# Optimization experiments

Hardware: AMD Instinct MI355X
Metric: run time of the kernel (lower is better)

Reference implementation:

```python
import jax, jax.numpy as jnp
import numpy as np

TEMPERATURE = 0.07
BASE_TEMPERATURE = 0.07


def setup_inputs() -> dict:
    key = jax.random.key(0)
    k1, k2 = jax.random.split(key)
    N, D = 8192, 512
    features = jax.random.normal(k1, (N, D), dtype=jnp.float32)
    labels = jax.random.randint(k2, (N,), 0, 64, dtype=jnp.int64 if jax.config.jax_enable_x64 else jnp.int32)
    return {"features": features, "labels": labels, "rotation_multiplier": 2}


def reference(features, labels, rotation_multiplier):
    k = int(rotation_multiplier)
    N = features.shape[0]
    B = N // k
    # L2-normalize rows (torch F.normalize clamps norm at eps=1e-12)
    norm = jnp.maximum(jnp.linalg.norm(features, axis=1, keepdims=True), 1e-12)
    f = features / norm
    sim = jnp.matmul(f, f.T) / TEMPERATURE  # [N, N]

    # block positive mask: groups of k rows share a label; compare group labels
    lab = labels.reshape(B, k)[:, 0]  # [B]
    same = lab[:, None] == lab[None, :]  # [B, B]
    mask = jnp.repeat(jnp.repeat(same, k, axis=0), k, axis=1)  # [N, N]
    eye = jnp.eye(N, dtype=bool)
    mask = mask & ~eye

    # stable masked log-softmax with diagonal removed from denominator
    logits_max = jax.lax.stop_gradient(jnp.max(sim, axis=1, keepdims=True))
    logits = sim - logits_max
    exp_logits = jnp.exp(logits)
    denom = exp_logits.sum(axis=1, keepdims=True) - jnp.diagonal(exp_logits)[:, None] + 1e-8
    log_prob = logits - jnp.log(denom)

    mask_f = mask.astype(logits.dtype)
    mask_sum = mask_f.sum(axis=1)  # [N]
    valid = mask_sum > 0
    mean_log_prob_pos = (log_prob * mask_f).sum(axis=1) / jnp.maximum(mask_sum, 1.0)
    per_sample = -(TEMPERATURE / BASE_TEMPERATURE) * mean_log_prob_pos
    n_valid = valid.sum().astype(logits.dtype)
    loss = jnp.where(valid, per_sample, 0.0).sum() / jnp.maximum(n_valid, 1.0)
    return loss
```

## Files before the change

kernel.cpp:

```cpp
#include <hip/hip_runtime.h>
#include <hip/hip_bf16.h>

#define TEMP_INV 14.285714285714286f
#define FSCALE 16.0f
#define T1S (TEMP_INV / 256.0f)

typedef __attribute__((ext_vector_type(4))) float f32x4;

#define ASYNC_COPY16(gp, lp)                                                  \
  __builtin_amdgcn_global_load_lds(                                           \
      (__attribute__((address_space(1))) const void*)(gp),                    \
      (__attribute__((address_space(3))) void*)(lp), 16, 0, 0)

__global__ __launch_bounds__(256) void norm_label_k(const float* __restrict__ feat,
                                                    uchar* __restrict__ fq,
                                                    const int* __restrict__ labels,
                                                    const int* __restrict__ kptr,
                                                    int* __restrict__ glab,
                                                    int* __restrict__ cnt,
                                                    float* __restrict__ gacc,
                                                    int* __restrict__ dcnt,
                                                    int N, int D) {
  const int row = (blockIdx.x * 256 + threadIdx.x) >> 6;
  const int lane = threadIdx.x & 63;
  if (row < N) {
    const float4* fr = (const float4*)(feat + (size_t)row * D);
    float4 v0 = fr[lane * 2];
    float4 v1 = fr[lane * 2 + 1];
    float ss = v0.x * v0.x + v0.y * v0.y + v0.z * v0.z + v0.w * v0.w +
               v1.x * v1.x + v1.y * v1.y + v1.z * v1.z + v1.w * v1.w;
    #pragma unroll
    for (int off = 32; off; off >>= 1) ss += __shfl_xor(ss, off, 64);
    const float inv = FSCALE / fmaxf(sqrtf(ss), 1e-12f);
    int w0 = 0, w1 = 0;
    w0 = __builtin_amdgcn_cvt_pk_fp8_f32(v0.x * inv, v0.y * inv, w0, false);
    w0 = __builtin_amdgcn_cvt_pk_fp8_f32(v0.z * inv, v0.w * inv, w0, true);
    w1 = __builtin_amdgcn_cvt_pk_fp8_f32(v1.x * inv, v1.y * inv, w1, false);
    w1 = __builtin_amdgcn_cvt_pk_fp8_f32(v1.z * inv, v1.w * inv, w1, true);
    uint2 o; o.x = (uint)w0; o.y = (uint)w1;
    *(uint2*)(fq + (size_t)row * D + lane * 8) = o;
  }
  if (blockIdx.x == 0) {
    const int k = *kptr;
    const int B = N / k;
    __shared__ int h[64];
    const int t = threadIdx.x;
    if (t < 2) gacc[t] = 0.f;
    if (t == 2) *dcnt = 0;
    if (t < 64) h[t] = 0;
    __syncthreads();
    for (int b = t; b < B; b += 256) {
      int lb = labels[(size_t)b * k];
      if (lb >= 0 && lb < 64) atomicAdd(&h[lb], 1);
    }
    __syncthreads();
    if (t < 64) cnt[t] = h[t];
    for (int i = t; i < N; i += 256) glab[i] = labels[(size_t)(i / k) * k];
  }
}

__global__ __launch_bounds__(256, 4) void gemm_k(const uchar* __restrict__ fq,
                                                 const int* __restrict__ glab,
                                                 float* __restrict__ part,
                                                 int N, int D) {
  __shared__ uchar As[128 * 128];
  __shared__ uchar Bs[128 * 128];
  const int t = threadIdx.x;
  const int lane = t & 63;
  const int wid = t >> 6;
  const int wrow = wid >> 1, wcol = wid & 1;
  const int quad = lane >> 4, l15 = lane & 15;

  const int nb = N / 128;
  const int total = nb * (nb + 1) / 2;
  int gidx = blockIdx.x;
  if ((total & 7) == 0) {
    const int per = total >> 3;
    gidx = (blockIdx.x & 7) * per + (blockIdx.x >> 3);
  }
  int idx = gidx, bi = 0;
  while (idx >= nb - bi) { idx -= nb - bi; bi++; }
  const int bj = bi + idx;
  const int i0 = bi * 128, j0 = bj * 128;
  const bool diagblk = (bi == bj);

  f32x4 acc[4][4];
  #pragma unroll
  for (int mi = 0; mi < 4; mi++)
    #pragma unroll
    for (int ni = 0; ni < 4; ni++) {
      f32x4 z = {0.f, 0.f, 0.f, 0.f};
      acc[mi][ni] = z;
    }

  uchar* sb = (wid < 2) ? As : Bs;
  const int rbase = (wid & 1) * 64;
  const int rowstart = ((wid < 2) ? i0 : j0) + rbase;
  const int lrow = lane >> 3;
  const int lch = lane & 7;

  const int h8 = (quad & 1) * 8;
  const int cq = quad >> 1;

  for (int kb = 0; kb < D; kb += 128) {
    __syncthreads();
    #pragma unroll
    for (int i = 0; i < 8; i++) {
      const int rl = 8 * i + lrow;
      const int cg = lch ^ (rl & 7);
      ASYNC_COPY16(fq + (size_t)(rowstart + rl) * D + kb + cg * 16,
                   sb + (rbase + 8 * i) * 128);
    }
    __syncthreads();
    #pragma unroll
    for (int s = 0; s < 4; s++) {
      const int c16 = s * 2 + cq;
      long a[4], b[4];
      #pragma unroll
      for (int mi = 0; mi < 4; mi++) {
        const int r = wrow * 64 + mi * 16 + l15;
        a[mi] = *(const long*)&As[r * 128 + ((c16 ^ (r & 7)) << 4) + h8];
      }
      #pragma unroll
      for (int ni = 0; ni < 4; ni++) {
        const int r = wcol * 64 + ni * 16 + l15;
        b[ni] = *(const long*)&Bs[r * 128 + ((c16 ^ (r & 7)) << 4) + h8];
      }
      #pragma unroll
      for (int mi = 0; mi < 4; mi++)
        #pragma unroll
        for (int ni = 0; ni < 4; ni++)
          acc[mi][ni] = __builtin_amdgcn_mfma_f32_16x16x32_fp8_fp8(a[mi], b[ni], acc[mi][ni], 0, 0, 0);
    }
  }

  __syncthreads();
  float* sf = (float*)As;
  const int colbase = j0 + wcol * 64 + l15;
  int clab[4];
  #pragma unroll
  for (int ni = 0; ni < 4; ni++) clab[ni] = glab[colbase + ni * 16];

  float colE[4] = {0.f, 0.f, 0.f, 0.f};
  float colP[4] = {0.f, 0.f, 0.f, 0.f};

  #pragma unroll
  for (int mi = 0; mi < 4; mi++) {
    const int lrw = wrow * 64 + mi * 16 + quad * 4;
    #pragma unroll
    for (int r = 0; r < 4; r++) {
      const int row = i0 + lrw + r;
      const int rlab = glab[row];
      float Ssum = 0.f, Psum = 0.f;
      #pragma unroll
      for (int ni = 0; ni < 4; ni++) {
        const int col = colbase + ni * 16;
        const float val = acc[mi][ni][r];
        const float lg = fmaf(val, T1S, -TEMP_INV);
        const bool diag = diagblk && (row == col);
        const float e = diag ? 0.f : __expf(lg);
        const float pm = (!diag && rlab == clab[ni]) ? lg : 0.f;
        Ssum += e; Psum += pm;
        colE[ni] += e; colP[ni] += pm;
      }
      #pragma unroll
      for (int off = 8; off; off >>= 1) {
        Ssum += __shfl_xor(Ssum, off, 64);
        Psum += __shfl_xor(Psum, off, 64);
      }
      if (l15 == 0) {
        sf[wcol * 128 + lrw + r]       = Ssum;
        sf[256 + wcol * 128 + lrw + r] = Psum;
      }
    }
  }
  if (!diagblk) {
    #pragma unroll
    for (int ni = 0; ni < 4; ni++) {
      float e = colE[ni];
      float p = colP[ni];
      e += __shfl_xor(e, 16, 64);
      e += __shfl_xor(e, 32, 64);
      p += __shfl_xor(p, 16, 64);
      p += __shfl_xor(p, 32, 64);
      const int lcol = wcol * 64 + ni * 16 + l15;
      if (quad == 0) {
        sf[512 + wrow * 128 + lcol] = e;
        sf[768 + wrow * 128 + lcol] = p;
      }
    }
  }
  __syncthreads();
  float* dst = part + (size_t)gidx * 512;
  if (t < 128) {
    dst[t]       = sf[t] + sf[128 + t];
    dst[128 + t] = sf[256 + t] + sf[384 + t];
  } else if (!diagblk) {
    const int u = t - 128;
    dst[256 + u] = sf[512 + u] + sf[640 + u];
    dst[384 + u] = sf[768 + u] + sf[896 + u];
  }
}

__global__ __launch_bounds__(128) void reduce_loss_k(const float* __restrict__ part,
                                                     const int* __restrict__ glab,
                                                     const int* __restrict__ cnt,
                                                     const int* __restrict__ kptr,
                                                     float* __restrict__ gacc,
                                                     int* __restrict__ dcnt,
                                                     float* __restrict__ out, int N) {
  const int nb = N / 128;
  const int b = blockIdx.x;
  const int t = threadIdx.x;
  const int i = b * 128 + t;
  float S = 0.f, P = 0.f;
  const int base = b * nb - b * (b - 1) / 2;
  for (int bj = b; bj < nb; bj++) {
    const float* p = part + (size_t)(base + bj - b) * 512;
    S += p[t];
    P += p[128 + t];
  }
  for (int bi = 0; bi < b; bi++) {
    const int idx = bi * nb - bi * (bi - 1) / 2 + (b - bi);
    const float* p = part + (size_t)idx * 512;
    S += p[256 + t];
    P += p[384 + t];
  }
  const int k = *kptr;
  const int np = cnt[glab[i]] * k - 1;
  float l = 0.f, v = 0.f;
  if (np > 0) {
    l = -(P - (float)np * logf(S + 1e-8f)) / (float)np;
    v = 1.f;
  }
  #pragma unroll
  for (int off = 32; off; off >>= 1) {
    l += __shfl_xor(l, off, 64);
    v += __shfl_xor(v, off, 64);
  }
  __shared__ float sl[2], sv[2];
  if ((t & 63) == 0) { sl[t >> 6] = l; sv[t >> 6] = v; }
  __syncthreads();
  if (t == 0) {
    atomicAdd(&gacc[0], sl[0] + sl[1]);
    atomicAdd(&gacc[1], sv[0] + sv[1]);
    __threadfence();
    const int prev = atomicAdd(dcnt, 1);
    if (prev == (int)gridDim.x - 1) {
      const float L = atomicAdd(&gacc[0], 0.f);
      const float V = atomicAdd(&gacc[1], 0.f);
      out[0] = L / fmaxf(V, 1.f);
    }
  }
}

extern "C" void kernel_launch(void* const* d_in, const int* in_sizes, int n_in,
                              void* d_out, int out_size, void* d_ws, size_t ws_size,
                              hipStream_t stream) {
  const float* feat = (const float*)d_in[0];
  const int* labels = (const int*)d_in[1];
  const int* kptr   = (const int*)d_in[2];
  const int N = in_sizes[1];
  const int D = in_sizes[0] / N;

  const int nb = N / 128;
  const int total = nb * (nb + 1) / 2;

  char* ws = (char*)d_ws;
  uchar* fq = (uchar*)ws;
  size_t off = (size_t)N * D;
  float* part = (float*)(ws + off); off += (size_t)total * 512 * sizeof(float);
  int* glab   = (int*)(ws + off);   off += (size_t)N * sizeof(int);
  int* cnt    = (int*)(ws + off);   off += 64 * sizeof(int);
  float* gacc = (float*)(ws + off); off += 2 * sizeof(float);
  int* dcnt   = (int*)(ws + off);   off += sizeof(int);

  norm_label_k<<<(N + 3) / 4, 256, 0, stream>>>(feat, fq, labels, kptr, glab, cnt,
                                                gacc, dcnt, N, D);
  gemm_k<<<total, 256, 0, stream>>>(fq, glab, part, N, D);
  reduce_loss_k<<<nb, 128, 0, stream>>>(part, glab, cnt, kptr, gacc, dcnt,
                                        (float*)d_out, N);
}
```

Measured before the change: 152.4 us.

## Double-buffer GEMM K-loop with async LDS prefetch of 64-wide chunks

Splits the shared-memory A/B tiles into two 64-byte-wide K buffers and restructures the K loop into eight fixed iterations. The next chunk is loaded asynchronously via global_load_lds while MFMAs run on the current chunk. This removes one barrier per step and is meant to hide global-load latency behind compute. The iteration count is now hardcoded for D=512, and the swizzle is reworked for the narrower rows.

```diff
diff --git a/kernel.cpp b/kernel.cpp
--- a/kernel.cpp
+++ b/kernel.cpp
@@ -8,7 +8,7 @@
 typedef __attribute__((ext_vector_type(4))) float f32x4;
 
 #define ASYNC_COPY16(gp, lp)                                                  \
-  __builtin_amdgcn_global_load_lds(                                           \
+  __builtin_amdgcn_global_load_lds(                                          \
       (__attribute__((address_space(1))) const void*)(gp),                    \
       (__attribute__((address_space(3))) void*)(lp), 16, 0, 0)
 
@@ -63,8 +63,8 @@
                                                  const int* __restrict__ glab,
                                                  float* __restrict__ part,
                                                  int N, int D) {
-  __shared__ uchar As[128 * 128];
-  __shared__ uchar Bs[128 * 128];
+  __shared__ uchar As[2][128 * 64];
+  __shared__ uchar Bs[2][128 * 64];
   const int t = threadIdx.x;
   const int lane = t & 63;
   const int wid = t >> 6;
@@ -93,38 +93,43 @@
       acc[mi][ni] = z;
     }
 
-  uchar* sb = (wid < 2) ? As : Bs;
+  const bool stA = wid < 2;
   const int rbase = (wid & 1) * 64;
-  const int rowstart = ((wid < 2) ? i0 : j0) + rbase;
-  const int lrow = lane >> 3;
-  const int lch = lane & 7;
-
-  const int h8 = (quad & 1) * 8;
-  const int cq = quad >> 1;
-
-  for (int kb = 0; kb < D; kb += 128) {
+  const int rowstart = (stA ? i0 : j0) + rbase;
+  const int lr = lane >> 2;
+  const int lch = lane & 3;
+  const uchar* gbase = fq + (size_t)rowstart * D + (size_t)lr * D +
+                       ((lch ^ (lr & 3)) << 4);
+
+  #define ISSUE_DMA(buf, kb)                                                  \
+    {                                                                         \
+      uchar* db = (stA ? As[buf] : Bs[buf]) + rbase * 64;                     \
+      _Pragma("unroll")                                                       \
+      for (int g = 0; g < 4; g++)                                             \
+        ASYNC_COPY16(gbase + (size_t)(g * 16) * D + (kb),                     \
+                     db + g * 16 * 64);                                       \
+    }
+
+  ISSUE_DMA(0, 0)
+  #pragma unroll
+  for (int it = 0; it < 8; it++) {
+    const int buf = it & 1;
     __syncthreads();
-    #pragma unroll
-    for (int i = 0; i < 8; i++) {
-      const int rl = 8 * i + lrow;
-      const int cg = lch ^ (rl & 7);
-      ASYNC_COPY16(fq + (size_t)(rowstart + rl) * D + kb + cg * 16,
-                   sb + (rbase + 8 * i) * 128);
-    }
-    __syncthreads();
-    #pragma unroll
-    for (int s = 0; s < 4; s++) {
-      const int c16 = s * 2 + cq;
+    if (it < 7) ISSUE_DMA(buf ^ 1, (it + 1) * 64)
+    #pragma unroll
+    for (int s2 = 0; s2 < 2; s2++) {
+      const int c = s2 * 2 + (quad >> 1);
+      const int h8 = (quad & 1) * 8;
       long a[4], b[4];
       #pragma unroll
       for (int mi = 0; mi < 4; mi++) {
         const int r = wrow * 64 + mi * 16 + l15;
-        a[mi] = *(const long*)&As[r * 128 + ((c16 ^ (r & 7)) << 4) + h8];
+        a[mi] = *(const long*)&As[buf][r * 64 + ((c ^ (r & 3)) << 4) + h8];
       }
       #pragma unroll
       for (int ni = 0; ni < 4; ni++) {
         const int r = wcol * 64 + ni * 16 + l15;
-        b[ni] = *(const long*)&Bs[r * 128 + ((c16 ^ (r & 7)) << 4) + h8];
+        b[ni] = *(const long*)&Bs[buf][r * 64 + ((c ^ (r & 3)) << 4) + h8];
       }
       #pragma unroll
       for (int mi = 0; mi < 4; mi++)
@@ -135,7 +140,7 @@
   }
 
   __syncthreads();
-  float* sf = (float*)As;
+  float* sf = (float*)&As[0][0];
   const int colbase = j0 + wcol * 64 + l15;
   int clab[4];
   #pragma unroll
```

Measured after the change: 163.9 us. +7.6%, slower.
